# Kernel tuning notes

Measured on AMD Instinct MI355X. Metric: run time of the kernel, lower is better.

Reference implementation:

```python
import jax, jax.numpy as jnp
import numpy as np

NUM_HEADS = 16
NUM_KV_HEADS = 4
ROPE_THETA = 10000.0


def apply_rope(x, position_ids, theta):
    # x: [B, S, h, d]; position_ids: [B, S]
    d = x.shape[-1]
    freqs = 1.0 / theta ** (jnp.arange(0, d, 2, dtype=jnp.float32) / d)  # [d/2]
    angles = position_ids.astype(jnp.float32)[..., None] * freqs          # [B, S, d/2]
    cos = jnp.cos(angles)[:, :, None, :]                                  # [B, S, 1, d/2]
    sin = jnp.sin(angles)[:, :, None, :]
    xr = x.astype(jnp.float32).reshape(*x.shape[:-1], d // 2, 2)
    x0, x1 = xr[..., 0], xr[..., 1]
    o0 = x0 * cos - x1 * sin
    o1 = x0 * sin + x1 * cos
    out = jnp.stack((o0, o1), axis=-1).reshape(*x.shape)
    return out.astype(x.dtype)


def setup_inputs() -> dict:
    key = jax.random.key(0)
    k0, k1, k2, k3, k4 = jax.random.split(key, 5)
    B, S, H = 1, 2048, 2048
    Hkv = H // (NUM_HEADS // NUM_KV_HEADS)  # 512
    init_scale = 0.02 / np.sqrt(H)
    return {
        "hidden_states": jax.random.normal(k0, (B, S, H), jnp.float32),
        "attention_mask": jnp.ones((B, S), jnp.int32),
        "segment_ids": jnp.zeros((B, S), jnp.int32),
        "position_ids": jnp.broadcast_to(jnp.arange(S, dtype=jnp.int32)[None], (B, S)),
        "Wq": jax.random.normal(k1, (H, H), jnp.float32) * init_scale,
        "Wk": jax.random.normal(k2, (H, Hkv), jnp.float32) * init_scale,
        "Wv": jax.random.normal(k3, (H, Hkv), jnp.float32) * init_scale,
        "Wo": jax.random.normal(k4, (H, H), jnp.float32) * init_scale,
    }


def reference(hidden_states, attention_mask, segment_ids, position_ids, Wq, Wk, Wv, Wo):
    B, S, H = hidden_states.shape
    nh, nkv = NUM_HEADS, NUM_KV_HEADS
    g = nh // nkv
    hd = H // nh

    xq = (hidden_states @ Wq).reshape(B, S, nh, hd)
    xk = (hidden_states @ Wk).reshape(B, S, nkv, hd)
    xv = (hidden_states @ Wv).reshape(B, S, nkv, hd)
    # GQA repeat: 'b s (h d) -> b s (h g) d' == repeat each kv head g times contiguously
    xk = jnp.repeat(xk, g, axis=2)  # [B, S, nh, hd]
    xv = jnp.repeat(xv, g, axis=2)

    xq = apply_rope(xq, position_ids, ROPE_THETA)
    xk = apply_rope(xk, position_ids, ROPE_THETA)

    # masks: causal AND padding AND segment
    causal = jnp.tril(jnp.ones((S, S), dtype=bool))[None, None]            # [1,1,S,S]
    pad = (attention_mask > 0)[:, None, None, :]                            # [B,1,1,S]
    seg = (segment_ids[:, :, None] == segment_ids[:, None, :])[:, None]     # [B,1,S,S]
    mask = causal & pad & seg                                               # [B,1,S,S]

    scale = 1.0 / np.sqrt(hd)
    logits = jnp.einsum("bqhd,bkhd->bhqk", xq.astype(jnp.float32), xk.astype(jnp.float32)) * scale
    logits = jnp.where(mask, logits, jnp.finfo(jnp.float32).min)
    probs = jax.nn.softmax(logits, axis=-1).astype(xv.dtype)
    attn = jnp.einsum("bhqk,bkhd->bqhd", probs, xv)                         # [B,S,nh,hd]

    out = attn.reshape(B, S, H) @ Wo
    return out
```

## Files before the change

kernel.cpp:

```cpp
#include <hip/hip_runtime.h>
#include <hip/hip_bf16.h>
#include <stdint.h>
#include <math.h>

#define SS 2048
#define HH 2048
#define NH 16
#define NKV 4
#define HD 128
#define HKV 512
#define NQKV 3072

typedef __bf16 bf16x8 __attribute__((ext_vector_type(8)));
typedef float f32x4 __attribute__((ext_vector_type(4)));

static_assert(sizeof(bf16x8) == 16, "bf16x8 must be 16B");

__device__ __forceinline__ void async_ld16(const void* gp, void* lp) {
  __builtin_amdgcn_global_load_lds(
      (const __attribute__((address_space(1))) unsigned int*)(uintptr_t)gp,
      (__attribute__((address_space(3))) unsigned int*)(uintptr_t)lp,
      16, 0, 0);
}

__device__ __forceinline__ unsigned short f2bu(float f) {
  __hip_bfloat16 b = __float2bfloat16(f);
  return *reinterpret_cast<unsigned short*>(&b);
}

__global__ __launch_bounds__(256) void k_prep1(
    const float* __restrict__ X, const float* __restrict__ Wq, const float* __restrict__ Wk,
    const float* __restrict__ Wv, const float* __restrict__ Wo,
    const int* __restrict__ amv, const int* __restrict__ seg, int* __restrict__ kseg,
    float2* __restrict__ rtab,
    __hip_bfloat16* __restrict__ Xb, __hip_bfloat16* __restrict__ WqT,
    __hip_bfloat16* __restrict__ WkT, __hip_bfloat16* __restrict__ WvT,
    __hip_bfloat16* __restrict__ WoT) {
  __shared__ __align__(16) __hip_bfloat16 t2[64 * 72];
  int b = blockIdx.x;
  int t = threadIdx.y * 32 + threadIdx.x;
  if (b < 4096) {
    int i = b * 256 + t;
    float4 v = ((const float4*)X)[i];
    ushort4 o;
    o.x = f2bu(v.x); o.y = f2bu(v.y); o.z = f2bu(v.z); o.w = f2bu(v.w);
    ((ushort4*)Xb)[i] = o;
    return;
  }
  b -= 4096;
  if (b >= 2568) {
    int i = (b - 2568) * 256 + t;
    int p = i >> 6, f = i & 63;
    const float L2T_D64 = 0.20762050593046837f;
    float freq = exp2f(-L2T_D64 * (float)f);
    float sn, cs;
    sincosf((float)p * freq, &sn, &cs);
    rtab[i] = make_float2(sn, cs);
    return;
  }
  if (b >= 2560) {
    int i = (b - 2560) * 256 + t;
    kseg[i] = (amv[i] > 0) ? seg[i] : 0x7fffffff;
    return;
  }
  const float* src; __hip_bfloat16* dst; int xtiles;
  if (b < 1024)      { src = Wq; dst = WqT; xtiles = 32; }
  else if (b < 2048) { src = Wo; dst = WoT; xtiles = 32; b -= 1024; }
  else if (b < 2304) { src = Wk; dst = WkT; xtiles = 8;  b -= 2048; }
  else               { src = Wv; dst = WvT; xtiles = 8;  b -= 2304; }
  const int C = xtiles * 64;
  int bx = (b % xtiles) * 64;
  int by = (b / xtiles) * 64;
#pragma unroll
  for (int i = 0; i < 4; i++) {
    int idx = i * 256 + t;
    int r = idx >> 4, c4 = (idx & 15) * 4;
    float4 v = *(const float4*)(src + (size_t)(by + r) * C + bx + c4);
    t2[(c4 + 0) * 72 + r] = __float2bfloat16(v.x);
    t2[(c4 + 1) * 72 + r] = __float2bfloat16(v.y);
    t2[(c4 + 2) * 72 + r] = __float2bfloat16(v.z);
    t2[(c4 + 3) * 72 + r] = __float2bfloat16(v.w);
  }
  __syncthreads();
#pragma unroll
  for (int i = 0; i < 2; i++) {
    int idx = i * 256 + t;
    int rr = idx >> 3, cc = (idx & 7) * 8;
    *(bf16x8*)(dst + (size_t)(bx + rr) * HH + by + cc) =
        *(const bf16x8*)(&t2[rr * 72 + cc]);
  }
}

__global__ __launch_bounds__(256, 2) void k_gemm_qkv(
    const __hip_bfloat16* __restrict__ A, const __hip_bfloat16* __restrict__ B,
    __hip_bfloat16* __restrict__ Qb, __hip_bfloat16* __restrict__ Kb,
    __hip_bfloat16* __restrict__ Vt, const int* __restrict__ pos,
    const float2* __restrict__ rtab) {
  __shared__ __align__(16) __hip_bfloat16 sA[2][128 * 64];
  __shared__ __align__(16) __hip_bfloat16 sB[2][96 * 64];
  const int tid = threadIdx.x;
  const int lane = tid & 63;
  const int wave = tid >> 6;
  const int lid = blockIdx.x;
  const int swz = (lid & 7) * 64 + (lid >> 3);
  const int bm = (swz >> 5) * 128;
  const int bn = (swz & 31) * 96;
  const int wm = (wave & 1) * 64;
  const int wn = (wave >> 1) * 48;
  const int am = lane & 15;
  const int ch = lane >> 4;

  f32x4 acc[4][3] = {};

  auto stage = [&](int p, int k0) {
#pragma unroll
    for (int q = 0; q < 4; q++) {
      int c = q * 256 + tid;
      int row = c >> 3, kp = c & 7;
      int col = (kp ^ (row & 7)) * 8;
      async_ld16(A + (size_t)(bm + row) * HH + k0 + col, (char*)&sA[p][0] + c * 16);
    }
#pragma unroll
    for (int q = 0; q < 3; q++) {
      int c = q * 256 + tid;
      int row = c >> 3, kp = c & 7;
      int col = (kp ^ (row & 7)) * 8;
      async_ld16(B + (size_t)(bn + row) * HH + k0 + col, (char*)&sB[p][0] + c * 16);
    }
  };
  auto compute = [&](int p) {
#pragma unroll
    for (int kb = 0; kb < 2; kb++) {
      bf16x8 a[4], b[3];
#pragma unroll
      for (int i = 0; i < 4; i++) {
        int row = wm + i * 16 + am;
        a[i] = *(const bf16x8*)(&sA[p][0] + row * 64 + (((kb * 4 + ch) ^ (row & 7)) * 8));
      }
#pragma unroll
      for (int j = 0; j < 3; j++) {
        int row = wn + j * 16 + am;
        b[j] = *(const bf16x8*)(&sB[p][0] + row * 64 + (((kb * 4 + ch) ^ (row & 7)) * 8));
      }
#pragma unroll
      for (int i = 0; i < 4; i++)
#pragma unroll
        for (int j = 0; j < 3; j++)
          acc[i][j] = __builtin_amdgcn_mfma_f32_16x16x32_bf16(a[i], b[j], acc[i][j], 0, 0, 0);
    }
  };

  stage(0, 0);
  int cur = 0;
  for (int t = 0; t < 32; ++t) {
    if (t + 1 < 32) {
      stage(cur ^ 1, (t + 1) * 64);
      asm volatile("s_waitcnt vmcnt(7)" ::: "memory");
    } else {
      asm volatile("s_waitcnt vmcnt(0)" ::: "memory");
    }
    asm volatile("s_barrier" ::: "memory");
    compute(cur);
    asm volatile("s_barrier" ::: "memory");
    cur ^= 1;
  }

  const float SCLQ = 0.08838834764831845f * 1.4426950408889634f;
  const float sgn = (am & 1) ? 1.0f : -1.0f;
  int pint[4][4];
#pragma unroll
  for (int i = 0; i < 4; i++)
#pragma unroll
    for (int r = 0; r < 4; r++)
      pint[i][r] = pos[bm + wm + i * 16 + ch * 4 + r];
#pragma unroll
  for (int j = 0; j < 3; j++) {
    const int colbase = bn + wn + j * 16;
    const int col = colbase + am;
    if (colbase >= HH + HKV) {
      int lc = col - (HH + HKV);
#pragma unroll
      for (int i = 0; i < 4; i++) {
        int row = bm + wm + i * 16 + ch * 4;
        ushort4 o;
        o.x = f2bu(acc[i][j][0]); o.y = f2bu(acc[i][j][1]);
        o.z = f2bu(acc[i][j][2]); o.w = f2bu(acc[i][j][3]);
        *(ushort4*)(Vt + (size_t)lc * SS + row) = o;
      }
    } else {
      const bool isQ = (colbase < HH);
      int lc = isQ ? col : (col - HH);
      int fidx = (lc >> 1) & 63;
#pragma unroll
      for (int i = 0; i < 4; i++)
#pragma unroll
        for (int r = 0; r < 4; r++) {
          float v = acc[i][j][r];
          float px = __shfl_xor(v, 1, 64);
          float2 sc = rtab[pint[i][r] * 64 + fidx];
          float o = v * sc.y + sgn * px * sc.x;
          int row = bm + wm + i * 16 + ch * 4 + r;
          if (isQ) Qb[(size_t)row * HH + col] = __float2bfloat16(o * SCLQ);
          else     Kb[(size_t)row * HKV + lc] = __float2bfloat16(o);
        }
    }
  }
}

__global__ __launch_bounds__(256, 3) void k_gemm_out(
    const __hip_bfloat16* __restrict__ A, const __hip_bfloat16* __restrict__ B,
    float* __restrict__ C) {
  __shared__ __align__(16) __hip_bfloat16 sA0[64 * 64];
  __shared__ __align__(16) __hip_bfloat16 sB0[128 * 64];
  __shared__ __align__(16) __hip_bfloat16 sA1[64 * 64];
  __shared__ __align__(16) __hip_bfloat16 sB1[128 * 64];
  const int tid = threadIdx.x;
  const int lane = tid & 63;
  const int wave = tid >> 6;
  const int bm = blockIdx.y * 64;
  const int bn = blockIdx.x * 128;
  const int wm = (wave & 1) * 32;
  const int wn = (wave >> 1) * 64;
  const int am = lane & 15;
  const int ch = lane >> 4;

  f32x4 acc[2][4] = {};

  auto stage = [&](__hip_bfloat16* sA, __hip_bfloat16* sB, int k0) {
#pragma unroll
    for (int q = 0; q < 2; q++) {
      int c = q * 256 + tid;
      int row = c >> 3, kp = c & 7;
      int col = (kp ^ (row & 7)) * 8;
      async_ld16(A + (size_t)(bm + row) * HH + k0 + col, (char*)sA + c * 16);
    }
#pragma unroll
    for (int q = 0; q < 4; q++) {
      int c = q * 256 + tid;
      int row = c >> 3, kp = c & 7;
      int col = (kp ^ (row & 7)) * 8;
      async_ld16(B + (size_t)(bn + row) * HH + k0 + col, (char*)sB + c * 16);
    }
  };
  auto compute = [&](const __hip_bfloat16* sA, const __hip_bfloat16* sB) {
#pragma unroll
    for (int kb = 0; kb < 2; kb++) {
      bf16x8 a[2], b[4];
#pragma unroll
      for (int i = 0; i < 2; i++) {
        int row = wm + i * 16 + am;
        a[i] = *(const bf16x8*)(sA + row * 64 + (((kb * 4 + ch) ^ (row & 7)) * 8));
      }
#pragma unroll
      for (int j = 0; j < 4; j++) {
        int row = wn + j * 16 + am;
        b[j] = *(const bf16x8*)(sB + row * 64 + (((kb * 4 + ch) ^ (row & 7)) * 8));
      }
#pragma unroll
      for (int i = 0; i < 2; i++)
#pragma unroll
        for (int j = 0; j < 4; j++)
          acc[i][j] = __builtin_amdgcn_mfma_f32_16x16x32_bf16(a[i], b[j], acc[i][j], 0, 0, 0);
    }
  };

  stage(sA0, sB0, 0);
  int k0 = 0;
  while (true) {
    __syncthreads();
    if (k0 + 64 < HH) stage(sA1, sB1, k0 + 64);
    compute(sA0, sB0);
    k0 += 64; if (k0 >= HH) break;
    __syncthreads();
    if (k0 + 64 < HH) stage(sA0, sB0, k0 + 64);
    compute(sA1, sB1);
    k0 += 64; if (k0 >= HH) break;
  }

#pragma unroll
  for (int i = 0; i < 2; i++)
#pragma unroll
    for (int j = 0; j < 4; j++)
#pragma unroll
      for (int r = 0; r < 4; r++) {
        int row = bm + wm + i * 16 + ch * 4 + r;
        int col = bn + wn + j * 16 + am;
        C[(size_t)row * HH + col] = acc[i][j][r];
      }
}

__global__ __launch_bounds__(256, 4) void k_attn(
    const __hip_bfloat16* __restrict__ Qb,
    const __hip_bfloat16* __restrict__ Kb,
    const __hip_bfloat16* __restrict__ Vt,
    const int* __restrict__ seg,
    const int* __restrict__ kseg,
    float* __restrict__ Obuf,
    float* __restrict__ Lbuf) {
  __shared__ __align__(16) __hip_bfloat16 sK[2][32 * 128];
  __shared__ __align__(16) __hip_bfloat16 sV[2][128 * 32];
  __shared__ __align__(16) __hip_bfloat16 sPall[4][16 * 32];

  const int bid = blockIdx.x;
  const int r4 = bid >> 8;
  const int s = (bid & 255) >> 3;
  const int t4 = bid & 7;
  int qtb = (r4 & 2) ? ((s + 16) & 31) : s;
  const int qt = (r4 & 1) ? (31 - qtb) : qtb;
  const int h = (t4 >> 1) * 4 + r4;
  const int half = t4 & 1;
  const int T = 2 * (qt + 1);
  const int n0 = qt + 1;
  const int kt0 = half ? n0 : 0;
  const int kt1 = half ? T : n0;

  const int kvh = h >> 2;
  const int tid = threadIdx.x, lane = tid & 63, w = tid >> 6;
  const int am = lane & 15, ch = lane >> 4;
  const int qrow0 = qt * 64 + w * 16;
  char* sP = (char*)&sPall[w][0];

  bf16x8 qf[4];
#pragma unroll
  for (int ks = 0; ks < 4; ks++)
    qf[ks] = *(const bf16x8*)(Qb + (size_t)(qrow0 + am) * HH + h * HD + ks * 32 + ch * 8);

  int segq[4];
#pragma unroll
  for (int r = 0; r < 4; r++) segq[r] = seg[qrow0 + ch * 4 + r];
  const int q0 = seg[qrow0];
  const bool quni = __all((segq[0] == q0) && (segq[1] == q0) &&
                          (segq[2] == q0) && (segq[3] == q0));

  f32x4 o_acc[8] = {};
  float l_s[4] = {0.f, 0.f, 0.f, 0.f};

  auto stage = [&](int kt, int p) {
#pragma unroll
    for (int q = 0; q < 2; q++) {
      int c = q * 256 + tid;
      int row = c >> 4, kp = c & 15;
      int col = (kp ^ (row & 15)) * 8;
      async_ld16(Kb + (size_t)(kt * 32 + row) * HKV + kvh * 128 + col, (char*)sK[p] + c * 16);
    }
#pragma unroll
    for (int q = 0; q < 2; q++) {
      int c = q * 256 + tid;
      int row = c >> 2, kp = c & 3;
      int col = (kp ^ ((row >> 1) & 3)) * 8;
      async_ld16(Vt + (size_t)(kvh * 128 + row) * SS + kt * 32 + col, (char*)sV[p] + c * 16);
    }
  };

  stage(kt0, 0);
  for (int kt = kt0; kt < kt1; kt++) {
    const int p = (kt - kt0) & 1;
    const int kbase = kt * 32;
    const bool skip = (kbase > qrow0 + 15);
    __syncthreads();

    int kinfo[2];
    if (!skip) {
#pragma unroll
      for (int jt = 0; jt < 2; jt++) kinfo[jt] = kseg[kbase + jt * 16 + am];
    }
    if (kt + 1 < kt1) stage(kt + 1, p ^ 1);
    if (!skip) {
      f32x4 sacc[2] = {};
      __builtin_amdgcn_s_setprio(1);
#pragma unroll
      for (int ks = 0; ks < 4; ks++)
#pragma unroll
        for (int jt = 0; jt < 2; jt++) {
          bf16x8 kf = *(const bf16x8*)(sK[p] + (jt * 16 + am) * 128 + (((ks * 4 + ch) ^ am) * 8));
          sacc[jt] = __builtin_amdgcn_mfma_f32_16x16x32_bf16(qf[ks], kf, sacc[jt], 0, 0, 0);
        }
      __builtin_amdgcn_s_setprio(0);

      const bool needc = (kbase + 31 > qrow0);
      const bool fast = quni && !needc &&
          __all((kinfo[0] == q0) && (kinfo[1] == q0));

      if (fast) {
#pragma unroll
        for (int jt = 0; jt < 2; jt++)
#pragma unroll
          for (int r = 0; r < 4; r++) {
            float pv = exp2f(sacc[jt][r] - 8.0f);
            l_s[r] += pv;
            int row = ch * 4 + r;
            int chunk = (jt * 2 + (am >> 3)) ^ ch;
            *(__hip_bfloat16*)(sP + row * 64 + chunk * 16 + (am & 7) * 2) =
                __float2bfloat16(pv);
          }
      } else {
#pragma unroll
        for (int jt = 0; jt < 2; jt++) {
          int kk = kbase + jt * 16 + am;
#pragma unroll
          for (int r = 0; r < 4; r++) {
            int qrow = qrow0 + ch * 4 + r;
            bool ok = (kinfo[jt] == segq[r]) && (kk <= qrow);
            float pv = ok ? exp2f(sacc[jt][r] - 8.0f) : 0.0f;
            l_s[r] += pv;
            int row = ch * 4 + r;
            int chunk = (jt * 2 + (am >> 3)) ^ ch;
            *(__hip_bfloat16*)(sP + row * 64 + chunk * 16 + (am & 7) * 2) =
                __float2bfloat16(pv);
          }
        }
      }

      __builtin_amdgcn_s_setprio(1);
      {
        bf16x8 pf = *(const bf16x8*)(sP + am * 64 + ((ch ^ ((am >> 2) & 3)) * 16));
#pragma unroll
        for (int jt = 0; jt < 8; jt++) {
          int vrow = jt * 16 + am;
          bf16x8 vf = *(const bf16x8*)(sV[p] + vrow * 32 + ((ch ^ ((vrow >> 1) & 3)) * 8));
          o_acc[jt] = __builtin_amdgcn_mfma_f32_16x16x32_bf16(pf, vf, o_acc[jt], 0, 0, 0);
        }
      }
      __builtin_amdgcn_s_setprio(0);
    }
  }

#pragma unroll
  for (int off = 1; off < 16; off <<= 1)
#pragma unroll
    for (int r = 0; r < 4; r++) l_s[r] += __shfl_xor(l_s[r], off, 64);
  if (am == 0)
#pragma unroll
    for (int r = 0; r < 4; r++)
      unsafeAtomicAdd(Lbuf + (size_t)(qrow0 + ch * 4 + r) * NH + h, l_s[r]);
#pragma unroll
  for (int jt = 0; jt < 8; jt++)
#pragma unroll
    for (int r = 0; r < 4; r++) {
      int row = qrow0 + ch * 4 + r;
      unsafeAtomicAdd(Obuf + (size_t)row * HH + h * HD + jt * 16 + am, o_acc[jt][r]);
    }
}

__global__ __launch_bounds__(256) void k_norm(
    const float* __restrict__ Obuf, const float* __restrict__ Lbuf,
    __hip_bfloat16* __restrict__ Ab) {
  int i = blockIdx.x * 256 + threadIdx.x;
  int s = i >> 9;
  int hIdx = (i & 511) >> 5;
  float inv = 1.0f / Lbuf[(size_t)s * NH + hIdx];
  float4 v = ((const float4*)Obuf)[i];
  ushort4 o;
  o.x = f2bu(v.x * inv); o.y = f2bu(v.y * inv);
  o.z = f2bu(v.z * inv); o.w = f2bu(v.w * inv);
  ((ushort4*)Ab)[i] = o;
}

extern "C" void kernel_launch(void* const* d_in, const int* in_sizes, int n_in,
                              void* d_out, int out_size, void* d_ws, size_t ws_size,
                              hipStream_t stream) {
  const float* X  = (const float*)d_in[0];
  const int* amv  = (const int*)d_in[1];
  const int* seg  = (const int*)d_in[2];
  const int* pos  = (const int*)d_in[3];
  const float* Wq = (const float*)d_in[4];
  const float* Wk = (const float*)d_in[5];
  const float* Wv = (const float*)d_in[6];
  const float* Wo = (const float*)d_in[7];
  float* out = (float*)d_out;

  char* ws = (char*)d_ws;
  size_t off = 0;
  auto alloc = [&](size_t bytes) { void* p = ws + off; off += (bytes + 255) & ~(size_t)255; return p; };
  __hip_bfloat16* Xb   = (__hip_bfloat16*)alloc((size_t)SS * HH * 2);
  __hip_bfloat16* WqT  = (__hip_bfloat16*)alloc((size_t)HH * HH * 2);
  __hip_bfloat16* WkT  = (__hip_bfloat16*)alloc((size_t)HKV * HH * 2);
  __hip_bfloat16* WvT  = (__hip_bfloat16*)alloc((size_t)HKV * HH * 2);
  __hip_bfloat16* WoT  = (__hip_bfloat16*)alloc((size_t)HH * HH * 2);
  __hip_bfloat16* Qb   = (__hip_bfloat16*)alloc((size_t)SS * HH * 2);
  __hip_bfloat16* Kb   = (__hip_bfloat16*)alloc((size_t)SS * HKV * 2);
  __hip_bfloat16* Vt   = (__hip_bfloat16*)alloc((size_t)HKV * SS * 2);
  __hip_bfloat16* Ab   = (__hip_bfloat16*)alloc((size_t)SS * HH * 2);
  float*          Obuf = (float*)alloc((size_t)SS * HH * 4);
  float*          Lbuf = (float*)alloc((size_t)SS * NH * 4);
  int*            kseg = (int*)alloc((size_t)SS * 4);
  float2*         rtab = (float2*)alloc((size_t)SS * 64 * 8);
  (void)WkT; (void)WvT;

  hipMemsetAsync(Obuf, 0, (size_t)SS * HH * 4 + ((size_t)SS * NH * 4 + 255 & ~(size_t)255), stream);
  k_prep1<<<dim3(7176), dim3(32, 8), 0, stream>>>(X, Wq, Wk, Wv, Wo, amv, seg, kseg, rtab,
                                                  Xb, WqT, WkT, WvT, WoT);
  k_gemm_qkv<<<dim3(512), 256, 0, stream>>>(Xb, WqT, Qb, Kb, Vt, pos, rtab);
  k_attn<<<dim3(1024), 256, 0, stream>>>(Qb, Kb, Vt, seg, kseg, Obuf, Lbuf);
  k_norm<<<dim3(SS * HH / 4 / 256), 256, 0, stream>>>(Obuf, Lbuf, Ab);
  k_gemm_out<<<dim3(HH / 128, SS / 64), 256, 0, stream>>>(Ab, WoT, out);
}
```

Before: 219.0 us.

## Use partial vmcnt waits with explicit barriers to overlap next-tile loads

Both the GEMM main loop and the attention K/V loop now issue the next tile's async global-to-LDS loads first. They then wait only until the previous tile's loads have landed, using vmcnt(6) instead of the full drain implied by __syncthreads. Explicit s_barrier calls before and after compute protect buffer reuse. This lets the prefetch for tile t+1 stay in flight while tile t is computed. It relies on the load count per stage being exactly 6 and on the kseg load counting toward vmcnt, so a miscount could cause a race. The kseg load is also now unconditional.

```diff
diff --git a/kernel.cpp b/kernel.cpp
--- a/kernel.cpp
+++ b/kernel.cpp
@@ -265,16 +265,20 @@
   };
 
   stage(sA0, sB0, 0);
-  int k0 = 0;
-  while (true) {
-    __syncthreads();
-    if (k0 + 64 < HH) stage(sA1, sB1, k0 + 64);
-    compute(sA0, sB0);
-    k0 += 64; if (k0 >= HH) break;
-    __syncthreads();
-    if (k0 + 64 < HH) stage(sA0, sB0, k0 + 64);
-    compute(sA1, sB1);
-    k0 += 64; if (k0 >= HH) break;
+  __hip_bfloat16 *cA = sA0, *cB = sB0, *nA = sA1, *nB = sB1;
+  for (int t = 0; t < 32; ++t) {
+    if (t + 1 < 32) {
+      stage(nA, nB, (t + 1) * 64);
+      asm volatile("s_waitcnt vmcnt(6)" ::: "memory");
+    } else {
+      asm volatile("s_waitcnt vmcnt(0)" ::: "memory");
+    }
+    asm volatile("s_barrier" ::: "memory");
+    compute(cA, cB);
+    asm volatile("s_barrier" ::: "memory");
+    __hip_bfloat16* tp;
+    tp = cA; cA = nA; nA = tp;
+    tp = cB; cB = nB; nB = tp;
   }
 
 #pragma unroll
@@ -357,14 +361,19 @@
     const int p = (kt - kt0) & 1;
     const int kbase = kt * 32;
     const bool skip = (kbase > qrow0 + 15);
-    __syncthreads();
 
     int kinfo[2];
-    if (!skip) {
-#pragma unroll
-      for (int jt = 0; jt < 2; jt++) kinfo[jt] = kseg[kbase + jt * 16 + am];
-    }
-    if (kt + 1 < kt1) stage(kt + 1, p ^ 1);
+#pragma unroll
+    for (int jt = 0; jt < 2; jt++) kinfo[jt] = kseg[kbase + jt * 16 + am];
+
+    if (kt + 1 < kt1) {
+      stage(kt + 1, p ^ 1);
+      asm volatile("s_waitcnt vmcnt(6)" ::: "memory");
+    } else {
+      asm volatile("s_waitcnt vmcnt(0)" ::: "memory");
+    }
+    asm volatile("s_barrier" ::: "memory");
+
     if (!skip) {
       f32x4 sacc[2] = {};
       __builtin_amdgcn_s_setprio(1);
@@ -423,6 +432,7 @@
       }
       __builtin_amdgcn_s_setprio(0);
     }
+    asm volatile("s_barrier" ::: "memory");
   }
 
 #pragma unroll
```

After: 219.8 us. No clear change (+0.4%).

## Fuse softmax normalization into output GEMM and fold buffer zeroing into prep

Applied to the files above, without the earlier changes.

The separate normalization kernel is removed. The output GEMM now loads the fp32 attention accumulator directly, scales each row by the reciprocal of its per-head softmax sum, converts to bf16 and writes it into shared memory. The zeroing of Obuf and Lbuf moves from a memset into extra blocks of the prep kernel, which relies on Lbuf sitting directly after Obuf in the workspace. This drops a full read and write of the intermediate activation and one launch. In exchange the GEMM's A-tile loads become synchronous fp32 loads that are re-read by every column block, in place of async bf16 loads straight to LDS.

```diff
diff --git a/kernel.cpp b/kernel.cpp
--- a/kernel.cpp
+++ b/kernel.cpp
@@ -32,7 +32,7 @@
     const float* __restrict__ X, const float* __restrict__ Wq, const float* __restrict__ Wk,
     const float* __restrict__ Wv, const float* __restrict__ Wo,
     const int* __restrict__ amv, const int* __restrict__ seg, int* __restrict__ kseg,
-    float2* __restrict__ rtab,
+    float2* __restrict__ rtab, float* __restrict__ Obuf,
     __hip_bfloat16* __restrict__ Xb, __hip_bfloat16* __restrict__ WqT,
     __hip_bfloat16* __restrict__ WkT, __hip_bfloat16* __restrict__ WvT,
     __hip_bfloat16* __restrict__ WoT) {
@@ -48,6 +48,11 @@
     return;
   }
   b -= 4096;
+  if (b >= 3080) {
+    int i = (b - 3080) * 256 + t;
+    ((float4*)Obuf)[i] = make_float4(0.f, 0.f, 0.f, 0.f);
+    return;
+  }
   if (b >= 2568) {
     int i = (b - 2568) * 256 + t;
     int p = i >> 6, f = i & 63;
@@ -208,8 +213,8 @@
 }
 
 __global__ __launch_bounds__(256, 3) void k_gemm_out(
-    const __hip_bfloat16* __restrict__ A, const __hip_bfloat16* __restrict__ B,
-    float* __restrict__ C) {
+    const float* __restrict__ Obuf, const float* __restrict__ Lbuf,
+    const __hip_bfloat16* __restrict__ B, float* __restrict__ C) {
   __shared__ __align__(16) __hip_bfloat16 sA0[64 * 64];
   __shared__ __align__(16) __hip_bfloat16 sB0[128 * 64];
   __shared__ __align__(16) __hip_bfloat16 sA1[64 * 64];
@@ -226,13 +231,23 @@
 
   f32x4 acc[2][4] = {};
 
-  auto stage = [&](__hip_bfloat16* sA, __hip_bfloat16* sB, int k0) {
+  auto stage = [&](__hip_bfloat16* sA, __hip_bfloat16* sB, int t) {
+    const int k0 = t * 64;
+    const int hd_head = t >> 1;
 #pragma unroll
     for (int q = 0; q < 2; q++) {
       int c = q * 256 + tid;
       int row = c >> 3, kp = c & 7;
       int col = (kp ^ (row & 7)) * 8;
-      async_ld16(A + (size_t)(bm + row) * HH + k0 + col, (char*)sA + c * 16);
+      float inv = 1.0f / Lbuf[(size_t)(bm + row) * NH + hd_head];
+      const float4* src = (const float4*)(Obuf + (size_t)(bm + row) * HH + k0 + col);
+      float4 v0 = src[0], v1 = src[1];
+      int4 w;
+      w.x = (int)f2bu(v0.x * inv) | ((int)f2bu(v0.y * inv) << 16);
+      w.y = (int)f2bu(v0.z * inv) | ((int)f2bu(v0.w * inv) << 16);
+      w.z = (int)f2bu(v1.x * inv) | ((int)f2bu(v1.y * inv) << 16);
+      w.w = (int)f2bu(v1.z * inv) | ((int)f2bu(v1.w * inv) << 16);
+      *(int4*)((char*)sA + c * 16) = w;
     }
 #pragma unroll
     for (int q = 0; q < 4; q++) {
@@ -265,16 +280,16 @@
   };
 
   stage(sA0, sB0, 0);
-  int k0 = 0;
+  int t = 0;
   while (true) {
     __syncthreads();
-    if (k0 + 64 < HH) stage(sA1, sB1, k0 + 64);
+    if (t + 1 < 32) stage(sA1, sB1, t + 1);
     compute(sA0, sB0);
-    k0 += 64; if (k0 >= HH) break;
+    ++t; if (t >= 32) break;
     __syncthreads();
-    if (k0 + 64 < HH) stage(sA0, sB0, k0 + 64);
+    if (t + 1 < 32) stage(sA0, sB0, t + 1);
     compute(sA1, sB1);
-    k0 += 64; if (k0 >= HH) break;
+    ++t; if (t >= 32) break;
   }
 
 #pragma unroll
@@ -442,20 +457,6 @@
     }
 }
 
-__global__ __launch_bounds__(256) void k_norm(
-    const float* __restrict__ Obuf, const float* __restrict__ Lbuf,
-    __hip_bfloat16* __restrict__ Ab) {
-  int i = blockIdx.x * 256 + threadIdx.x;
-  int s = i >> 9;
-  int hIdx = (i & 511) >> 5;
-  float inv = 1.0f / Lbuf[(size_t)s * NH + hIdx];
-  float4 v = ((const float4*)Obuf)[i];
-  ushort4 o;
-  o.x = f2bu(v.x * inv); o.y = f2bu(v.y * inv);
-  o.z = f2bu(v.z * inv); o.w = f2bu(v.w * inv);
-  ((ushort4*)Ab)[i] = o;
-}
-
 extern "C" void kernel_launch(void* const* d_in, const int* in_sizes, int n_in,
                               void* d_out, int out_size, void* d_ws, size_t ws_size,
                               hipStream_t stream) {
@@ -480,18 +481,15 @@
   __hip_bfloat16* Qb   = (__hip_bfloat16*)alloc((size_t)SS * HH * 2);
   __hip_bfloat16* Kb   = (__hip_bfloat16*)alloc((size_t)SS * HKV * 2);
   __hip_bfloat16* Vt   = (__hip_bfloat16*)alloc((size_t)HKV * SS * 2);
-  __hip_bfloat16* Ab   = (__hip_bfloat16*)alloc((size_t)SS * HH * 2);
   float*          Obuf = (float*)alloc((size_t)SS * HH * 4);
   float*          Lbuf = (float*)alloc((size_t)SS * NH * 4);
   int*            kseg = (int*)alloc((size_t)SS * 4);
   float2*         rtab = (float2*)alloc((size_t)SS * 64 * 8);
   (void)WkT; (void)WvT;
 
-  hipMemsetAsync(Obuf, 0, (size_t)SS * HH * 4 + ((size_t)SS * NH * 4 + 255 & ~(size_t)255), stream);
-  k_prep1<<<dim3(7176), dim3(32, 8), 0, stream>>>(X, Wq, Wk, Wv, Wo, amv, seg, kseg, rtab,
-                                                  Xb, WqT, WkT, WvT, WoT);
+  k_prep1<<<dim3(11304), dim3(32, 8), 0, stream>>>(X, Wq, Wk, Wv, Wo, amv, seg, kseg,
+                                                   rtab, Obuf, Xb, WqT, WkT, WvT, WoT);
   k_gemm_qkv<<<dim3(512), 256, 0, stream>>>(Xb, WqT, Qb, Kb, Vt, pos, rtab);
   k_attn<<<dim3(1024), 256, 0, stream>>>(Qb, Kb, Vt, seg, kseg, Obuf, Lbuf);
-  k_norm<<<dim3(SS * HH / 4 / 256), 256, 0, stream>>>(Obuf, Lbuf, Ab);
-  k_gemm_out<<<dim3(HH / 128, SS / 64), 256, 0, stream>>>(Ab, WoT, out);
-}
+  k_gemm_out<<<dim3(HH / 128, SS / 64), 256, 0, stream>>>(Obuf, Lbuf, WoT, out);
+}
```

Result: slower. 223.5 us (+2.1%).
